# Optimization experiments

Measured on AMD Instinct MI355X. Metric: run time of the kernel, lower is better.

## Reference

```python
import jax, jax.numpy as jnp
import numpy as np

NODE_DIM = 64
DEPTH = 2
N = 50000          # node_size
DEG = 24           # average degree
E = N * DEG        # triple_size = 1.2M edges
R = 500            # rel_size
FEAT = NODE_DIM * (DEPTH + 1)  # 192


def _l2norm(x, eps=1e-12):
    # torch F.normalize(p=2): x / max(||x||, eps)
    n = jnp.sqrt(jnp.sum(x * x, axis=-1, keepdims=True))
    return x / jnp.maximum(n, eps)


def setup_inputs() -> dict:
    key = jax.random.key(0)
    ks = jax.random.split(key, 8)
    features = jax.random.normal(ks[0], (N, NODE_DIM), jnp.float32)
    rel_emb = jax.random.normal(ks[1], (R, NODE_DIM), jnp.float32)
    # duplicate-free edge list, rows sorted (matches a coalesced sparse adj)
    rows = jnp.repeat(jnp.arange(N, dtype=jnp.int32), DEG)
    offs = jnp.tile(1 + jnp.arange(DEG, dtype=jnp.int32) * 7, N)
    cols = (rows + offs) % N
    adj = jnp.stack([rows, cols])  # [2, E]
    # sparse [E, R] triple->relation matrix: one relation per triple
    r_index = jnp.stack([jnp.arange(E, dtype=jnp.int32),
                         jax.random.randint(ks[2], (E,), 0, R, jnp.int32)])
    r_val = jax.random.uniform(ks[3], (E,), jnp.float32, 0.5, 1.5)
    # params (xavier-ish scales)
    proxy = jax.random.normal(ks[4], (64, FEAT), jnp.float32) * (1.0 / np.sqrt(FEAT))
    gate_w = jax.random.normal(ks[5], (FEAT, FEAT), jnp.float32) * (1.0 / np.sqrt(FEAT))
    gate_b = jnp.zeros((FEAT,), jnp.float32)
    attn_kernels = jax.random.normal(ks[6], (DEPTH, NODE_DIM), jnp.float32) * 0.1
    return {"features": features, "rel_emb": rel_emb, "proxy": proxy,
            "gate_w": gate_w, "gate_b": gate_b, "attn_kernels": attn_kernels,
            "adj": adj, "r_index": r_index, "r_val": r_val,
            "triple_size": E, "rel_size": R, "node_size": N}


def reference(features, rel_emb, proxy, gate_w, gate_b, attn_kernels,
              adj, r_index, r_val, triple_size, rel_size, node_size):
    feats = jnp.tanh(features)
    outs = [feats]
    dst = adj[0]  # rows: softmax / scatter-sum segment ids
    src = adj[1]  # cols: neighbor gather ids
    for l in range(attn_kernels.shape[0]):
        neighs = feats[src]                                  # [E, d] gather
        # sparse.mm(tri_rel, rel_emb): sum_k r_val * rel_emb[rel_id] per triple
        tri_rel = jax.ops.segment_sum(r_val[:, None] * rel_emb[r_index[1]],
                                      r_index[0], num_segments=triple_size)
        tri_rel = _l2norm(tri_rel)                           # [E, d]
        # relational reflection: h - 2 <h, r> r
        neighs = neighs - 2.0 * jnp.sum(neighs * tri_rel, axis=1, keepdims=True) * tri_rel
        att = jnp.einsum('ed,d->e', tri_rel, attn_kernels[l])  # [E]
        # sparse softmax over rows of adjacency (segment softmax over dst)
        m = jax.ops.segment_max(att, dst, num_segments=node_size)
        ex = jnp.exp(att - m[dst])
        denom = jax.ops.segment_sum(ex, dst, num_segments=node_size)
        w = ex / denom[dst]
        new_f = jax.ops.segment_sum(neighs * w[:, None], dst, num_segments=node_size)
        feats = jnp.tanh(new_f)
        outs.append(feats)
    outputs = jnp.concatenate(outs, axis=-1)                 # [N, feat]
    proxy_att = jax.nn.softmax(_l2norm(outputs) @ _l2norm(proxy).T, axis=-1)
    proxy_feature = outputs - proxy_att @ proxy
    gate = jax.nn.sigmoid(proxy_feature @ gate_w.T + gate_b)
    return gate * outputs + (1.0 - gate) * proxy_feature
```

## Files before the change

### kernel.cpp

```cpp
#include <hip/hip_runtime.h>
#include <hip/hip_bf16.h>
#include <cstdint>
#include <cstddef>

#define N_NODES 50000
#define DEG     24
#define NEDGE   (N_NODES*DEG)
#define RSZ     500
#define NDIM    64
#define FEATD   192

#define LSTR    200

#define LGRID   1568
#define LCHUNK  196

typedef short bf16x8 __attribute__((ext_vector_type(8)));
typedef float f32x4  __attribute__((ext_vector_type(4)));

__device__ __forceinline__ unsigned short f2bf(float f) {
    unsigned u = __builtin_bit_cast(unsigned, f);
    unsigned r = (u + 0x7fffu + ((u >> 16) & 1u)) >> 16;
    return (unsigned short)r;
}
__device__ __forceinline__ float bf2f(unsigned short s) {
    unsigned u = ((unsigned)s) << 16;
    return __builtin_bit_cast(float, u);
}
__device__ __forceinline__ float lo16(unsigned u) {
    return __builtin_bit_cast(float, u << 16);
}
__device__ __forceinline__ float hi16(unsigned u) {
    return __builtin_bit_cast(float, u & 0xFFFF0000u);
}
__device__ __forceinline__ float fast_tanh(float x) {
    float e = __expf(2.f * x);
    return 1.f - 2.f / (e + 1.f);
}

__global__ __launch_bounds__(256) void k_prep(const float* __restrict__ features,
                                              const float* __restrict__ rel_emb,
                                              const float* __restrict__ attn_k,
                                              const float* __restrict__ proxy,
                                              const float* __restrict__ gate_w,
                                              const int* __restrict__ src,
                                              const int* __restrict__ rel,
                                              unsigned short* __restrict__ fin0,
                                              float* __restrict__ reln,
                                              float* __restrict__ expdot,
                                              float* __restrict__ pninv,
                                              unsigned short* __restrict__ B1,
                                              unsigned short* __restrict__ B2,
                                              unsigned short* __restrict__ B3,
                                              unsigned int* __restrict__ pedge) {
    int b = blockIdx.x;
    if (b < 3125) {
        int t = b * 256 + threadIdx.x;
        int idx4 = t * 4;
        float4 f = *reinterpret_cast<const float4*>(features + idx4);
        uint2 w;
        w.x = (unsigned)f2bf(fast_tanh(f.x)) | ((unsigned)f2bf(fast_tanh(f.y)) << 16);
        w.y = (unsigned)f2bf(fast_tanh(f.z)) | ((unsigned)f2bf(fast_tanh(f.w)) << 16);
        *reinterpret_cast<uint2*>(fin0 + idx4) = w;
    } else if (b < 3250) {
        int lane = threadIdx.x & 63;
        int row = (b - 3125) * 4 + (threadIdx.x >> 6);
        float v = rel_emb[row * 64 + lane];
        float ss = v * v;
        for (int m = 1; m < 64; m <<= 1) ss += __shfl_xor(ss, m);
        float inv = 1.f / fmaxf(sqrtf(ss), 1e-12f);
        float rn = v * inv;
        reln[row * 64 + lane] = rn;
        float d0 = rn * attn_k[lane];
        float d1 = rn * attn_k[64 + lane];
        for (int m = 1; m < 64; m <<= 1) { d0 += __shfl_xor(d0, m); d1 += __shfl_xor(d1, m); }
        if (lane == 0) { expdot[row] = __expf(d0); expdot[RSZ + row] = __expf(d1); }
    } else if (b < 3266) {
        int lane = threadIdx.x & 63;
        int row = (b - 3250) * 4 + (threadIdx.x >> 6);
        const float* p = proxy + (size_t)row * FEATD;
        float a = p[lane], bb = p[64 + lane], c = p[128 + lane];
        float ss = a * a + bb * bb + c * c;
        for (int m = 1; m < 64; m <<= 1) ss += __shfl_xor(ss, m);
        if (lane == 0) pninv[row] = 1.f / fmaxf(sqrtf(ss), 1e-12f);
    } else if (b < 3506) {
        int idx = (b - 3266) * 256 + threadIdx.x;
        int j = idx & 7, lane = (idx >> 3) & 63;
        int t = idx >> 9;
        int lane16 = lane & 15, quad = lane >> 4;
        if (t < 24) {
            int kt = t >> 2, nt = t & 3;
            int k = kt * 32 + quad * 8 + j, n = nt * 16 + lane16;
            B1[idx] = f2bf(proxy[(size_t)n * FEATD + k]);
        } else if (t < 48) {
            int tt = t - 24, kt = tt / 12, nt = tt % 12;
            int k = kt * 32 + quad * 8 + j, n = nt * 16 + lane16;
            B2[idx - 12288] = f2bf(proxy[(size_t)k * FEATD + n]);
        } else {
            int tt = t - 48, kt = tt / 12, nt = tt % 12;
            int k = kt * 32 + quad * 8 + j, n = nt * 16 + lane16;
            B3[idx - 24576] = f2bf(gate_w[(size_t)n * FEATD + k]);
        }
    } else {
        int t = (b - 3506) * 256 + threadIdx.x;
        if (t < NEDGE / 4) {
            int4 s4 = *reinterpret_cast<const int4*>(src + t * 4);
            int4 r4 = *reinterpret_cast<const int4*>(rel + t * 4);
            uint4 o;
            o.x = (unsigned)s4.x | ((unsigned)r4.x << 16);
            o.y = (unsigned)s4.y | ((unsigned)r4.y << 16);
            o.z = (unsigned)s4.z | ((unsigned)r4.z << 16);
            o.w = (unsigned)s4.w | ((unsigned)r4.w << 16);
            *reinterpret_cast<uint4*>(pedge + t * 4) = o;
        }
    }
}

__global__ __launch_bounds__(256) void k_layer(const unsigned int* __restrict__ pedge,
                                               const float* __restrict__ reln,
                                               const float* __restrict__ expdot_l,
                                               const unsigned short* __restrict__ fin,
                                               unsigned short* __restrict__ fout) {
    int b = blockIdx.x;
    int lb = (b & 7) * LCHUNK + (b >> 3);
    int lane8 = threadIdx.x & 7;
    int node = lb * 32 + (threadIdx.x >> 3);
    if (node >= N_NODES) return;
    int ebase = node * DEG;
    unsigned pk[DEG];
#pragma unroll
    for (int k = 0; k < DEG; k++) pk[k] = pedge[ebase + k];
    float a0 = 0.f, a1 = 0.f, a2 = 0.f, a3 = 0.f;
    float a4 = 0.f, a5 = 0.f, a6 = 0.f, a7 = 0.f, den = 0.f;
#pragma unroll 4
    for (int k = 0; k < DEG; k++) {
        unsigned p = pk[k];
        int s = p & 0xFFFF;
        int r = p >> 16;
        float ex = expdot_l[r];
        const float* tp = reln + (size_t)r * 64 + lane8 * 8;
        float4 t0 = *reinterpret_cast<const float4*>(tp);
        float4 t1v = *reinterpret_cast<const float4*>(tp + 4);
        uint4 u = *reinterpret_cast<const uint4*>(fin + (size_t)s * 64 + lane8 * 8);
        float n0 = lo16(u.x), n1 = hi16(u.x), n2 = lo16(u.y), n3 = hi16(u.y);
        float n4 = lo16(u.z), n5 = hi16(u.z), n6 = lo16(u.w), n7 = hi16(u.w);
        float pd = t0.x * n0 + t0.y * n1 + t0.z * n2 + t0.w * n3
                 + t1v.x * n4 + t1v.y * n5 + t1v.z * n6 + t1v.w * n7;
        pd += __shfl_xor(pd, 1); pd += __shfl_xor(pd, 2); pd += __shfl_xor(pd, 4);
        float t1 = -2.f * pd * ex;
        a0 = fmaf(ex, n0, fmaf(t1, t0.x, a0));
        a1 = fmaf(ex, n1, fmaf(t1, t0.y, a1));
        a2 = fmaf(ex, n2, fmaf(t1, t0.z, a2));
        a3 = fmaf(ex, n3, fmaf(t1, t0.w, a3));
        a4 = fmaf(ex, n4, fmaf(t1, t1v.x, a4));
        a5 = fmaf(ex, n5, fmaf(t1, t1v.y, a5));
        a6 = fmaf(ex, n6, fmaf(t1, t1v.z, a6));
        a7 = fmaf(ex, n7, fmaf(t1, t1v.w, a7));
        den += ex;
    }
    float id = 1.f / den;
    uint4 w;
    w.x = (unsigned)f2bf(fast_tanh(a0 * id)) | ((unsigned)f2bf(fast_tanh(a1 * id)) << 16);
    w.y = (unsigned)f2bf(fast_tanh(a2 * id)) | ((unsigned)f2bf(fast_tanh(a3 * id)) << 16);
    w.z = (unsigned)f2bf(fast_tanh(a4 * id)) | ((unsigned)f2bf(fast_tanh(a5 * id)) << 16);
    w.w = (unsigned)f2bf(fast_tanh(a6 * id)) | ((unsigned)f2bf(fast_tanh(a7 * id)) << 16);
    *reinterpret_cast<uint4*>(fout + (size_t)node * 64 + lane8 * 8) = w;
}

__global__ __launch_bounds__(256) void k_gate(const unsigned short* __restrict__ fin0,
                                              const unsigned short* __restrict__ fin1,
                                              const unsigned short* __restrict__ fin2,
                                              const unsigned short* __restrict__ B1,
                                              const unsigned short* __restrict__ B2,
                                              const unsigned short* __restrict__ B3,
                                              const float* __restrict__ pninv,
                                              const float* __restrict__ gate_b,
                                              float* __restrict__ dout) {
    __shared__ unsigned short lds[4][16 * LSTR];
    int wv = threadIdx.x >> 6, lane = threadIdx.x & 63;
    int tile = blockIdx.x * 4 + wv;
    if (tile > N_NODES / 16 - 1) tile = N_NODES / 16 - 1;
    int row0 = tile * 16, lane16 = lane & 15, quad = lane >> 4;
    unsigned short* L = lds[wv];
    const unsigned short* fsel[3] = {fin0, fin1, fin2};

    float oreg[12][4];
#pragma unroll
    for (int nt = 0; nt < 12; nt++) {
        const unsigned short* f = fsel[nt >> 2];
#pragma unroll
        for (int r = 0; r < 4; r++)
            oreg[nt][r] = bf2f(f[(size_t)(row0 + quad * 4 + r) * 64 + (nt & 3) * 16 + lane16]);
    }

    bf16x8 af[6];
    float ss = 0.f;
#pragma unroll
    for (int kt = 0; kt < 6; kt++) {
        const unsigned short* f = fsel[kt >> 1];
        bf16x8 a = *reinterpret_cast<const bf16x8*>(f + (size_t)(row0 + lane16) * 64 + (kt & 1) * 32 + quad * 8);
        af[kt] = a;
#pragma unroll
        for (int i = 0; i < 8; i++) {
            float v = bf2f((unsigned short)a[i]);
            ss = fmaf(v, v, ss);
        }
    }
    ss += __shfl_xor(ss, 16); ss += __shfl_xor(ss, 32);
    float inv = 1.f / fmaxf(sqrtf(ss), 1e-12f);
    float pni[4];
#pragma unroll
    for (int nt = 0; nt < 4; nt++) pni[nt] = pninv[nt * 16 + lane16];
    f32x4 acc4[4];
#pragma unroll
    for (int nt = 0; nt < 4; nt++) acc4[nt] = (f32x4){0.f, 0.f, 0.f, 0.f};
#pragma unroll
    for (int kt = 0; kt < 6; kt++) {
#pragma unroll
        for (int nt = 0; nt < 4; nt++) {
            bf16x8 bfr = *reinterpret_cast<const bf16x8*>(B1 + ((size_t)(kt * 4 + nt) * 64 + lane) * 8);
            acc4[nt] = __builtin_amdgcn_mfma_f32_16x16x32_bf16(af[kt], bfr, acc4[nt], 0, 0, 0);
        }
    }
#pragma unroll
    for (int r = 0; r < 4; r++) {
        int rowloc = quad * 4 + r;
        float invr = __shfl(inv, rowloc);
        float e0 = __expf(acc4[0][r] * invr * pni[0]);
        float e1 = __expf(acc4[1][r] * invr * pni[1]);
        float e2 = __expf(acc4[2][r] * invr * pni[2]);
        float e3 = __expf(acc4[3][r] * invr * pni[3]);
        float s = e0 + e1 + e2 + e3;
        s += __shfl_xor(s, 1); s += __shfl_xor(s, 2);
        s += __shfl_xor(s, 4); s += __shfl_xor(s, 8);
        float rs = 1.f / s;
        L[rowloc * LSTR + lane16]      = f2bf(e0 * rs);
        L[rowloc * LSTR + 16 + lane16] = f2bf(e1 * rs);
        L[rowloc * LSTR + 32 + lane16] = f2bf(e2 * rs);
        L[rowloc * LSTR + 48 + lane16] = f2bf(e3 * rs);
    }
    __threadfence_block();

    f32x4 acc[12];
#pragma unroll
    for (int nt = 0; nt < 12; nt++) acc[nt] = (f32x4){0.f, 0.f, 0.f, 0.f};
#pragma unroll
    for (int kt = 0; kt < 2; kt++) {
        bf16x8 a = *reinterpret_cast<const bf16x8*>(L + lane16 * LSTR + kt * 32 + quad * 8);
#pragma unroll
        for (int nt = 0; nt < 12; nt++) {
            bf16x8 bfr = *reinterpret_cast<const bf16x8*>(B2 + ((size_t)(kt * 12 + nt) * 64 + lane) * 8);
            acc[nt] = __builtin_amdgcn_mfma_f32_16x16x32_bf16(a, bfr, acc[nt], 0, 0, 0);
        }
    }
    __threadfence_block();
#pragma unroll
    for (int nt = 0; nt < 12; nt++) {
#pragma unroll
        for (int r = 0; r < 4; r++) {
            int rowloc = quad * 4 + r;
            L[rowloc * LSTR + nt * 16 + lane16] = f2bf(oreg[nt][r] - acc[nt][r]);
        }
    }
    __threadfence_block();

#pragma unroll
    for (int nt = 0; nt < 12; nt++) acc[nt] = (f32x4){0.f, 0.f, 0.f, 0.f};
#pragma unroll
    for (int kt = 0; kt < 6; kt++) {
        bf16x8 a = *reinterpret_cast<const bf16x8*>(L + lane16 * LSTR + kt * 32 + quad * 8);
#pragma unroll
        for (int nt = 0; nt < 12; nt++) {
            bf16x8 bfr = *reinterpret_cast<const bf16x8*>(B3 + ((size_t)(kt * 12 + nt) * 64 + lane) * 8);
            acc[nt] = __builtin_amdgcn_mfma_f32_16x16x32_bf16(a, bfr, acc[nt], 0, 0, 0);
        }
    }

#pragma unroll
    for (int nt = 0; nt < 12; nt++) {
        float bias = gate_b[nt * 16 + lane16];
#pragma unroll
        for (int r = 0; r < 4; r++) {
            int rowloc = quad * 4 + r;
            size_t idx = (size_t)(row0 + rowloc) * FEATD + nt * 16 + lane16;
            float z = acc[nt][r] + bias;
            float g = 1.f / (1.f + __expf(-z));
            float pf = bf2f(L[rowloc * LSTR + nt * 16 + lane16]);
            dout[idx] = pf + g * (oreg[nt][r] - pf);
        }
    }
}

extern "C" void kernel_launch(void* const* d_in, const int* in_sizes, int n_in,
                              void* d_out, int out_size, void* d_ws, size_t ws_size,
                              hipStream_t stream) {
    (void)in_sizes; (void)n_in; (void)out_size; (void)ws_size;
    const float* features = (const float*)d_in[0];
    const float* rel_emb  = (const float*)d_in[1];
    const float* proxy    = (const float*)d_in[2];
    const float* gate_w   = (const float*)d_in[3];
    const float* gate_b   = (const float*)d_in[4];
    const float* attn_k   = (const float*)d_in[5];
    const int*   adj      = (const int*)d_in[6];
    const int*   r_index  = (const int*)d_in[7];

    unsigned short* fin0 = (unsigned short*)d_ws;
    unsigned short* fin1 = fin0 + (size_t)N_NODES * 64;
    unsigned short* fin2 = fin1 + (size_t)N_NODES * 64;
    float* reln    = (float*)(fin2 + (size_t)N_NODES * 64);
    float* expdot  = reln + RSZ * 64;
    float* pninv   = expdot + 2 * RSZ;
    unsigned short* B1 = (unsigned short*)(pninv + 64);
    unsigned short* B2 = B1 + 12288;
    unsigned short* B3 = B2 + 12288;
    unsigned int* pedge = (unsigned int*)(B3 + 36864);

    const int* src = adj + NEDGE;
    const int* rel = r_index + NEDGE;

    k_prep  <<<dim3(4678), dim3(256), 0, stream>>>(features, rel_emb, attn_k, proxy, gate_w,
                                                   src, rel, fin0, reln, expdot,
                                                   pninv, B1, B2, B3, pedge);
    k_layer <<<dim3(LGRID), dim3(256), 0, stream>>>(pedge, reln, expdot,       fin0, fin1);
    k_layer <<<dim3(LGRID), dim3(256), 0, stream>>>(pedge, reln, expdot + RSZ, fin1, fin2);
    k_gate  <<<dim3(782),  dim3(256), 0, stream>>>(fin0, fin1, fin2, B1, B2, B3, pninv,
                                                   gate_b, (float*)d_out);
}
```

Baseline: 186.8 us.

## Stage normalized relation table in LDS with persistent 1024-thread layer blocks

Adds a layer kernel that loads the 500x64 normalized relation embeddings and per-relation exp weights into shared memory (~138KB, padded stride) once per block, then processes 196 nodes per block with 256 large blocks. Relation lookups per edge hit LDS instead of global/L2. The large LDS allocation limits occupancy to one block per CU and adds a per-block table load; falls back to the old kernel if the attribute set fails.

New measurement: 183.0 us. 2.0% less time.

```diff
diff --git a/kernel.cpp b/kernel.cpp
--- a/kernel.cpp
+++ b/kernel.cpp
@@ -14,6 +14,10 @@
 
 #define LGRID   1568
 #define LCHUNK  196
+
+#define NPB     196
+#define SREL_STRIDE 68
+#define LAYER_LDS_BYTES ((RSZ*SREL_STRIDE + RSZ) * 4)
 
 typedef short bf16x8 __attribute__((ext_vector_type(8)));
 typedef float f32x4  __attribute__((ext_vector_type(4)));
@@ -116,6 +120,72 @@
     }
 }
 
+__global__ __launch_bounds__(1024) void k_layer_lds(const unsigned int* __restrict__ pedge,
+                                                    const float* __restrict__ reln,
+                                                    const float* __restrict__ expdot_l,
+                                                    const unsigned short* __restrict__ fin,
+                                                    unsigned short* __restrict__ fout) {
+    extern __shared__ float smem[];
+    float* srel = smem;
+    float* sexp = smem + RSZ * SREL_STRIDE;
+    {
+        const float4* s4 = reinterpret_cast<const float4*>(reln);
+        for (int i = threadIdx.x; i < RSZ * 16; i += 1024) {
+            int row = i >> 4, c4 = i & 15;
+            *reinterpret_cast<float4*>(srel + row * SREL_STRIDE + c4 * 4) = s4[i];
+        }
+        for (int i = threadIdx.x; i < RSZ; i += 1024) sexp[i] = expdot_l[i];
+    }
+    __syncthreads();
+    int b = blockIdx.x;
+    int lb = (b & 7) * 32 + (b >> 3);
+    int base = lb * NPB;
+    int lane8 = threadIdx.x & 7;
+    for (int local = threadIdx.x >> 3; local < NPB; local += 128) {
+        int node = base + local;
+        if (node >= N_NODES) break;
+        int ebase = node * DEG;
+        unsigned pk[DEG];
+#pragma unroll
+        for (int k = 0; k < DEG; k++) pk[k] = pedge[ebase + k];
+        float a0 = 0.f, a1 = 0.f, a2 = 0.f, a3 = 0.f;
+        float a4 = 0.f, a5 = 0.f, a6 = 0.f, a7 = 0.f, den = 0.f;
+#pragma unroll 2
+        for (int k = 0; k < DEG; k++) {
+            unsigned p = pk[k];
+            int s = p & 0xFFFF;
+            int r = p >> 16;
+            float ex = sexp[r];
+            const float* tp = srel + r * SREL_STRIDE + lane8 * 8;
+            float4 t0 = *reinterpret_cast<const float4*>(tp);
+            float4 t1v = *reinterpret_cast<const float4*>(tp + 4);
+            uint4 u = *reinterpret_cast<const uint4*>(fin + (size_t)s * 64 + lane8 * 8);
+            float n0 = lo16(u.x), n1 = hi16(u.x), n2 = lo16(u.y), n3 = hi16(u.y);
+            float n4 = lo16(u.z), n5 = hi16(u.z), n6 = lo16(u.w), n7 = hi16(u.w);
+            float pd = t0.x * n0 + t0.y * n1 + t0.z * n2 + t0.w * n3
+                     + t1v.x * n4 + t1v.y * n5 + t1v.z * n6 + t1v.w * n7;
+            pd += __shfl_xor(pd, 1); pd += __shfl_xor(pd, 2); pd += __shfl_xor(pd, 4);
+            float t1 = -2.f * pd * ex;
+            a0 = fmaf(ex, n0, fmaf(t1, t0.x, a0));
+            a1 = fmaf(ex, n1, fmaf(t1, t0.y, a1));
+            a2 = fmaf(ex, n2, fmaf(t1, t0.z, a2));
+            a3 = fmaf(ex, n3, fmaf(t1, t0.w, a3));
+            a4 = fmaf(ex, n4, fmaf(t1, t1v.x, a4));
+            a5 = fmaf(ex, n5, fmaf(t1, t1v.y, a5));
+            a6 = fmaf(ex, n6, fmaf(t1, t1v.z, a6));
+            a7 = fmaf(ex, n7, fmaf(t1, t1v.w, a7));
+            den += ex;
+        }
+        float id = 1.f / den;
+        uint4 w;
+        w.x = (unsigned)f2bf(fast_tanh(a0 * id)) | ((unsigned)f2bf(fast_tanh(a1 * id)) << 16);
+        w.y = (unsigned)f2bf(fast_tanh(a2 * id)) | ((unsigned)f2bf(fast_tanh(a3 * id)) << 16);
+        w.z = (unsigned)f2bf(fast_tanh(a4 * id)) | ((unsigned)f2bf(fast_tanh(a5 * id)) << 16);
+        w.w = (unsigned)f2bf(fast_tanh(a6 * id)) | ((unsigned)f2bf(fast_tanh(a7 * id)) << 16);
+        *reinterpret_cast<uint4*>(fout + (size_t)node * 64 + lane8 * 8) = w;
+    }
+}
+
 __global__ __launch_bounds__(256) void k_layer(const unsigned int* __restrict__ pedge,
                                                const float* __restrict__ reln,
                                                const float* __restrict__ expdot_l,
@@ -318,11 +388,24 @@
     const int* src = adj + NEDGE;
     const int* rel = r_index + NEDGE;
 
+    static int lds_mode = -1;
+    if (lds_mode < 0) {
+        hipError_t e = hipFuncSetAttribute((const void*)k_layer_lds,
+                                           hipFuncAttributeMaxDynamicSharedMemorySize,
+                                           LAYER_LDS_BYTES);
+        lds_mode = (e == hipSuccess) ? 1 : 0;
+    }
+
     k_prep  <<<dim3(4678), dim3(256), 0, stream>>>(features, rel_emb, attn_k, proxy, gate_w,
                                                    src, rel, fin0, reln, expdot,
                                                    pninv, B1, B2, B3, pedge);
-    k_layer <<<dim3(LGRID), dim3(256), 0, stream>>>(pedge, reln, expdot,       fin0, fin1);
-    k_layer <<<dim3(LGRID), dim3(256), 0, stream>>>(pedge, reln, expdot + RSZ, fin1, fin2);
+    if (lds_mode == 1) {
+        k_layer_lds <<<dim3(256), dim3(1024), LAYER_LDS_BYTES, stream>>>(pedge, reln, expdot,       fin0, fin1);
+        k_layer_lds <<<dim3(256), dim3(1024), LAYER_LDS_BYTES, stream>>>(pedge, reln, expdot + RSZ, fin1, fin2);
+    } else {
+        k_layer <<<dim3(LGRID), dim3(256), 0, stream>>>(pedge, reln, expdot,       fin0, fin1);
+        k_layer <<<dim3(LGRID), dim3(256), 0, stream>>>(pedge, reln, expdot + RSZ, fin1, fin2);
+    }
     k_gate  <<<dim3(782),  dim3(256), 0, stream>>>(fin0, fin1, fin2, B1, B2, B3, pninv,
                                                    gate_b, (float*)d_out);
 }
```

## Remap blocks XCD-aware across prep and gate kernels and batch B-fragment loads

Applied to the files above, without the earlier changes.

The features-to-bf16 part of the prep kernel now handles 32 nodes per block with a block-index swizzle of the form (b&7)*chunk + (b>>3). The edge-packing part and the gate kernel use the same kind of remap, so that blocks scheduled on the same XCD handle contiguous node ranges, matching the layer kernel's chunking and improving L2 locality. The gate kernel gets a launch-bounds occupancy hint, and its B-fragment global loads are batched before the MFMA chains to expose memory-level parallelism. The grids are resized to fit the new mapping. The batched loads raise register pressure, and the occupancy hint may force spills.

Result: no change. 184.3 us (-1.4%).

```diff
diff --git a/kernel.cpp b/kernel.cpp
--- a/kernel.cpp
+++ b/kernel.cpp
@@ -54,17 +54,24 @@
                                               unsigned short* __restrict__ B3,
                                               unsigned int* __restrict__ pedge) {
     int b = blockIdx.x;
-    if (b < 3125) {
-        int t = b * 256 + threadIdx.x;
-        int idx4 = t * 4;
-        float4 f = *reinterpret_cast<const float4*>(features + idx4);
-        uint2 w;
-        w.x = (unsigned)f2bf(fast_tanh(f.x)) | ((unsigned)f2bf(fast_tanh(f.y)) << 16);
-        w.y = (unsigned)f2bf(fast_tanh(f.z)) | ((unsigned)f2bf(fast_tanh(f.w)) << 16);
-        *reinterpret_cast<uint2*>(fin0 + idx4) = w;
-    } else if (b < 3250) {
+    if (b < 1568) {
+        int lb = (b & 7) * LCHUNK + (b >> 3);
+        int node = lb * 32 + ((int)threadIdx.x >> 3);
+        if (node < N_NODES) {
+            int d0 = ((int)threadIdx.x & 7) * 8;
+            const float* fp = features + (size_t)node * 64 + d0;
+            float4 f0 = *reinterpret_cast<const float4*>(fp);
+            float4 f1 = *reinterpret_cast<const float4*>(fp + 4);
+            uint4 w;
+            w.x = (unsigned)f2bf(fast_tanh(f0.x)) | ((unsigned)f2bf(fast_tanh(f0.y)) << 16);
+            w.y = (unsigned)f2bf(fast_tanh(f0.z)) | ((unsigned)f2bf(fast_tanh(f0.w)) << 16);
+            w.z = (unsigned)f2bf(fast_tanh(f1.x)) | ((unsigned)f2bf(fast_tanh(f1.y)) << 16);
+            w.w = (unsigned)f2bf(fast_tanh(f1.z)) | ((unsigned)f2bf(fast_tanh(f1.w)) << 16);
+            *reinterpret_cast<uint4*>(fin0 + (size_t)node * 64 + d0) = w;
+        }
+    } else if (b < 1693) {
         int lane = threadIdx.x & 63;
-        int row = (b - 3125) * 4 + (threadIdx.x >> 6);
+        int row = (b - 1568) * 4 + (threadIdx.x >> 6);
         float v = rel_emb[row * 64 + lane];
         float ss = v * v;
         for (int m = 1; m < 64; m <<= 1) ss += __shfl_xor(ss, m);
@@ -75,16 +82,16 @@
         float d1 = rn * attn_k[64 + lane];
         for (int m = 1; m < 64; m <<= 1) { d0 += __shfl_xor(d0, m); d1 += __shfl_xor(d1, m); }
         if (lane == 0) { expdot[row] = __expf(d0); expdot[RSZ + row] = __expf(d1); }
-    } else if (b < 3266) {
+    } else if (b < 1709) {
         int lane = threadIdx.x & 63;
-        int row = (b - 3250) * 4 + (threadIdx.x >> 6);
+        int row = (b - 1693) * 4 + (threadIdx.x >> 6);
         const float* p = proxy + (size_t)row * FEATD;
         float a = p[lane], bb = p[64 + lane], c = p[128 + lane];
         float ss = a * a + bb * bb + c * c;
         for (int m = 1; m < 64; m <<= 1) ss += __shfl_xor(ss, m);
         if (lane == 0) pninv[row] = 1.f / fmaxf(sqrtf(ss), 1e-12f);
-    } else if (b < 3506) {
-        int idx = (b - 3266) * 256 + threadIdx.x;
+    } else if (b < 1949) {
+        int idx = (b - 1709) * 256 + threadIdx.x;
         int j = idx & 7, lane = (idx >> 3) & 63;
         int t = idx >> 9;
         int lane16 = lane & 15, quad = lane >> 4;
@@ -102,7 +109,9 @@
             B3[idx - 24576] = f2bf(gate_w[(size_t)n * FEATD + k]);
         }
     } else {
-        int t = (b - 3506) * 256 + threadIdx.x;
+        int bb = b - 1949;
+        int lb = (bb & 7) * 147 + (bb >> 3);
+        int t = lb * 256 + (int)threadIdx.x;
         if (t < NEDGE / 4) {
             int4 s4 = *reinterpret_cast<const int4*>(src + t * 4);
             int4 r4 = *reinterpret_cast<const int4*>(rel + t * 4);
@@ -167,18 +176,20 @@
     *reinterpret_cast<uint4*>(fout + (size_t)node * 64 + lane8 * 8) = w;
 }
 
-__global__ __launch_bounds__(256) void k_gate(const unsigned short* __restrict__ fin0,
-                                              const unsigned short* __restrict__ fin1,
-                                              const unsigned short* __restrict__ fin2,
-                                              const unsigned short* __restrict__ B1,
-                                              const unsigned short* __restrict__ B2,
-                                              const unsigned short* __restrict__ B3,
-                                              const float* __restrict__ pninv,
-                                              const float* __restrict__ gate_b,
-                                              float* __restrict__ dout) {
+__global__ __launch_bounds__(256, 3) void k_gate(const unsigned short* __restrict__ fin0,
+                                                 const unsigned short* __restrict__ fin1,
+                                                 const unsigned short* __restrict__ fin2,
+                                                 const unsigned short* __restrict__ B1,
+                                                 const unsigned short* __restrict__ B2,
+                                                 const unsigned short* __restrict__ B3,
+                                                 const float* __restrict__ pninv,
+                                                 const float* __restrict__ gate_b,
+                                                 float* __restrict__ dout) {
     __shared__ unsigned short lds[4][16 * LSTR];
     int wv = threadIdx.x >> 6, lane = threadIdx.x & 63;
-    int tile = blockIdx.x * 4 + wv;
+    int b = blockIdx.x;
+    int lb = (b & 7) * 98 + (b >> 3);
+    int tile = lb * 4 + wv;
     if (tile > N_NODES / 16 - 1) tile = N_NODES / 16 - 1;
     int row0 = tile * 16, lane16 = lane & 15, quad = lane >> 4;
     unsigned short* L = lds[wv];
@@ -215,12 +226,18 @@
 #pragma unroll
     for (int nt = 0; nt < 4; nt++) acc4[nt] = (f32x4){0.f, 0.f, 0.f, 0.f};
 #pragma unroll
-    for (int kt = 0; kt < 6; kt++) {
-#pragma unroll
-        for (int nt = 0; nt < 4; nt++) {
-            bf16x8 bfr = *reinterpret_cast<const bf16x8*>(B1 + ((size_t)(kt * 4 + nt) * 64 + lane) * 8);
-            acc4[nt] = __builtin_amdgcn_mfma_f32_16x16x32_bf16(af[kt], bfr, acc4[nt], 0, 0, 0);
-        }
+    for (int ktp = 0; ktp < 3; ktp++) {
+        bf16x8 bb[8];
+#pragma unroll
+        for (int h = 0; h < 2; h++)
+#pragma unroll
+            for (int nt = 0; nt < 4; nt++)
+                bb[h * 4 + nt] = *reinterpret_cast<const bf16x8*>(B1 + ((size_t)((ktp * 2 + h) * 4 + nt) * 64 + lane) * 8);
+#pragma unroll
+        for (int h = 0; h < 2; h++)
+#pragma unroll
+            for (int nt = 0; nt < 4; nt++)
+                acc4[nt] = __builtin_amdgcn_mfma_f32_16x16x32_bf16(af[ktp * 2 + h], bb[h * 4 + nt], acc4[nt], 0, 0, 0);
     }
 #pragma unroll
     for (int r = 0; r < 4; r++) {
@@ -247,11 +264,13 @@
 #pragma unroll
     for (int kt = 0; kt < 2; kt++) {
         bf16x8 a = *reinterpret_cast<const bf16x8*>(L + lane16 * LSTR + kt * 32 + quad * 8);
-#pragma unroll
-        for (int nt = 0; nt < 12; nt++) {
-            bf16x8 bfr = *reinterpret_cast<const bf16x8*>(B2 + ((size_t)(kt * 12 + nt) * 64 + lane) * 8);
-            acc[nt] = __builtin_amdgcn_mfma_f32_16x16x32_bf16(a, bfr, acc[nt], 0, 0, 0);
-        }
+        bf16x8 bb[12];
+#pragma unroll
+        for (int nt = 0; nt < 12; nt++)
+            bb[nt] = *reinterpret_cast<const bf16x8*>(B2 + ((size_t)(kt * 12 + nt) * 64 + lane) * 8);
+#pragma unroll
+        for (int nt = 0; nt < 12; nt++)
+            acc[nt] = __builtin_amdgcn_mfma_f32_16x16x32_bf16(a, bb[nt], acc[nt], 0, 0, 0);
     }
     __threadfence_block();
 #pragma unroll
@@ -269,11 +288,13 @@
 #pragma unroll
     for (int kt = 0; kt < 6; kt++) {
         bf16x8 a = *reinterpret_cast<const bf16x8*>(L + lane16 * LSTR + kt * 32 + quad * 8);
-#pragma unroll
-        for (int nt = 0; nt < 12; nt++) {
-            bf16x8 bfr = *reinterpret_cast<const bf16x8*>(B3 + ((size_t)(kt * 12 + nt) * 64 + lane) * 8);
-            acc[nt] = __builtin_amdgcn_mfma_f32_16x16x32_bf16(a, bfr, acc[nt], 0, 0, 0);
-        }
+        bf16x8 bb[12];
+#pragma unroll
+        for (int nt = 0; nt < 12; nt++)
+            bb[nt] = *reinterpret_cast<const bf16x8*>(B3 + ((size_t)(kt * 12 + nt) * 64 + lane) * 8);
+#pragma unroll
+        for (int nt = 0; nt < 12; nt++)
+            acc[nt] = __builtin_amdgcn_mfma_f32_16x16x32_bf16(a, bb[nt], acc[nt], 0, 0, 0);
     }
 
 #pragma unroll
@@ -318,11 +339,11 @@
     const int* src = adj + NEDGE;
     const int* rel = r_index + NEDGE;
 
-    k_prep  <<<dim3(4678), dim3(256), 0, stream>>>(features, rel_emb, attn_k, proxy, gate_w,
+    k_prep  <<<dim3(3125), dim3(256), 0, stream>>>(features, rel_emb, attn_k, proxy, gate_w,
                                                    src, rel, fin0, reln, expdot,
                                                    pninv, B1, B2, B3, pedge);
     k_layer <<<dim3(LGRID), dim3(256), 0, stream>>>(pedge, reln, expdot,       fin0, fin1);
     k_layer <<<dim3(LGRID), dim3(256), 0, stream>>>(pedge, reln, expdot + RSZ, fin1, fin2);
-    k_gate  <<<dim3(782),  dim3(256), 0, stream>>>(fin0, fin1, fin2, B1, B2, B3, pninv,
+    k_gate  <<<dim3(784),  dim3(256), 0, stream>>>(fin0, fin1, fin2, B1, B2, B3, pninv,
                                                    gate_b, (float*)d_out);
 }
```

## Fuse both GNN layers into one persistent kernel with a grid barrier

Applied to the files above, without the earlier changes.

Merges the two per-layer launches into one persistent kernel of 784 blocks. Each block handles two node groups per layer, and a global atomic-counter barrier sits between the layers. The barrier counter is zeroed in the prep kernel. The gate kernel also batches its B-fragment loads ahead of the MFMA chains and gets launch-bound hints, meant to trim launch gaps and hide load latency. In exchange it relies on all 784 blocks being co-resident for the spin barrier (deadlock risk otherwise) and gives up the parallel slack of the larger grid.

Measured after the change: 370.0 us. +98.0%, slower.

```diff
diff --git a/kernel.cpp b/kernel.cpp
--- a/kernel.cpp
+++ b/kernel.cpp
@@ -12,7 +12,7 @@
 
 #define LSTR    200
 
-#define LGRID   1568
+#define NBLK    784
 #define LCHUNK  196
 
 typedef short bf16x8 __attribute__((ext_vector_type(8)));
@@ -52,8 +52,10 @@
                                               unsigned short* __restrict__ B1,
                                               unsigned short* __restrict__ B2,
                                               unsigned short* __restrict__ B3,
-                                              unsigned int* __restrict__ pedge) {
+                                              unsigned int* __restrict__ pedge,
+                                              unsigned int* __restrict__ bar) {
     int b = blockIdx.x;
+    if (b == 0 && threadIdx.x < 2) bar[threadIdx.x] = 0;
     if (b < 3125) {
         int t = b * 256 + threadIdx.x;
         int idx4 = t * 4;
@@ -116,15 +118,15 @@
     }
 }
 
-__global__ __launch_bounds__(256) void k_layer(const unsigned int* __restrict__ pedge,
-                                               const float* __restrict__ reln,
-                                               const float* __restrict__ expdot_l,
-                                               const unsigned short* __restrict__ fin,
-                                               unsigned short* __restrict__ fout) {
-    int b = blockIdx.x;
-    int lb = (b & 7) * LCHUNK + (b >> 3);
-    int lane8 = threadIdx.x & 7;
-    int node = lb * 32 + (threadIdx.x >> 3);
+__device__ __forceinline__ void layer_pass(int lg, int tid,
+                                           const unsigned int* __restrict__ pedge,
+                                           const float* __restrict__ reln,
+                                           const float* __restrict__ expdot_l,
+                                           const unsigned short* __restrict__ fin,
+                                           unsigned short* __restrict__ fout) {
+    int lb = (lg & 7) * LCHUNK + (lg >> 3);
+    int lane8 = tid & 7;
+    int node = lb * 32 + (tid >> 3);
     if (node >= N_NODES) return;
     int ebase = node * DEG;
     unsigned pk[DEG];
@@ -167,15 +169,38 @@
     *reinterpret_cast<uint4*>(fout + (size_t)node * 64 + lane8 * 8) = w;
 }
 
-__global__ __launch_bounds__(256) void k_gate(const unsigned short* __restrict__ fin0,
-                                              const unsigned short* __restrict__ fin1,
-                                              const unsigned short* __restrict__ fin2,
-                                              const unsigned short* __restrict__ B1,
-                                              const unsigned short* __restrict__ B2,
-                                              const unsigned short* __restrict__ B3,
-                                              const float* __restrict__ pninv,
-                                              const float* __restrict__ gate_b,
-                                              float* __restrict__ dout) {
+__global__ __launch_bounds__(256, 4) void k_layers(const unsigned int* __restrict__ pedge,
+                                                   const float* __restrict__ reln,
+                                                   const float* __restrict__ expdot,
+                                                   const unsigned short* __restrict__ fin0,
+                                                   unsigned short* __restrict__ fin1,
+                                                   unsigned short* __restrict__ fin2,
+                                                   unsigned int* bar) {
+    int tid = threadIdx.x;
+    int b = blockIdx.x;
+    layer_pass(b,        tid, pedge, reln, expdot, fin0, fin1);
+    layer_pass(b + NBLK, tid, pedge, reln, expdot, fin0, fin1);
+    __threadfence();
+    __syncthreads();
+    if (tid == 0) {
+        atomicAdd(bar, 1u);
+        while (atomicAdd(bar, 0u) < (unsigned)NBLK) __builtin_amdgcn_s_sleep(2);
+    }
+    __syncthreads();
+    __threadfence();
+    layer_pass(b,        tid, pedge, reln, expdot + RSZ, fin1, fin2);
+    layer_pass(b + NBLK, tid, pedge, reln, expdot + RSZ, fin1, fin2);
+}
+
+__global__ __launch_bounds__(256, 3) void k_gate(const unsigned short* __restrict__ fin0,
+                                                 const unsigned short* __restrict__ fin1,
+                                                 const unsigned short* __restrict__ fin2,
+                                                 const unsigned short* __restrict__ B1,
+                                                 const unsigned short* __restrict__ B2,
+                                                 const unsigned short* __restrict__ B3,
+                                                 const float* __restrict__ pninv,
+                                                 const float* __restrict__ gate_b,
+                                                 float* __restrict__ dout) {
     __shared__ unsigned short lds[4][16 * LSTR];
     int wv = threadIdx.x >> 6, lane = threadIdx.x & 63;
     int tile = blockIdx.x * 4 + wv;
@@ -215,12 +240,18 @@
 #pragma unroll
     for (int nt = 0; nt < 4; nt++) acc4[nt] = (f32x4){0.f, 0.f, 0.f, 0.f};
 #pragma unroll
-    for (int kt = 0; kt < 6; kt++) {
-#pragma unroll
-        for (int nt = 0; nt < 4; nt++) {
-            bf16x8 bfr = *reinterpret_cast<const bf16x8*>(B1 + ((size_t)(kt * 4 + nt) * 64 + lane) * 8);
-            acc4[nt] = __builtin_amdgcn_mfma_f32_16x16x32_bf16(af[kt], bfr, acc4[nt], 0, 0, 0);
-        }
+    for (int ktp = 0; ktp < 3; ktp++) {
+        bf16x8 bb[8];
+#pragma unroll
+        for (int h = 0; h < 2; h++)
+#pragma unroll
+            for (int nt = 0; nt < 4; nt++)
+                bb[h * 4 + nt] = *reinterpret_cast<const bf16x8*>(B1 + ((size_t)((ktp * 2 + h) * 4 + nt) * 64 + lane) * 8);
+#pragma unroll
+        for (int h = 0; h < 2; h++)
+#pragma unroll
+            for (int nt = 0; nt < 4; nt++)
+                acc4[nt] = __builtin_amdgcn_mfma_f32_16x16x32_bf16(af[ktp * 2 + h], bb[h * 4 + nt], acc4[nt], 0, 0, 0);
     }
 #pragma unroll
     for (int r = 0; r < 4; r++) {
@@ -247,11 +278,13 @@
 #pragma unroll
     for (int kt = 0; kt < 2; kt++) {
         bf16x8 a = *reinterpret_cast<const bf16x8*>(L + lane16 * LSTR + kt * 32 + quad * 8);
-#pragma unroll
-        for (int nt = 0; nt < 12; nt++) {
-            bf16x8 bfr = *reinterpret_cast<const bf16x8*>(B2 + ((size_t)(kt * 12 + nt) * 64 + lane) * 8);
-            acc[nt] = __builtin_amdgcn_mfma_f32_16x16x32_bf16(a, bfr, acc[nt], 0, 0, 0);
-        }
+        bf16x8 bb[12];
+#pragma unroll
+        for (int nt = 0; nt < 12; nt++)
+            bb[nt] = *reinterpret_cast<const bf16x8*>(B2 + ((size_t)(kt * 12 + nt) * 64 + lane) * 8);
+#pragma unroll
+        for (int nt = 0; nt < 12; nt++)
+            acc[nt] = __builtin_amdgcn_mfma_f32_16x16x32_bf16(a, bb[nt], acc[nt], 0, 0, 0);
     }
     __threadfence_block();
 #pragma unroll
@@ -269,11 +302,13 @@
 #pragma unroll
     for (int kt = 0; kt < 6; kt++) {
         bf16x8 a = *reinterpret_cast<const bf16x8*>(L + lane16 * LSTR + kt * 32 + quad * 8);
-#pragma unroll
-        for (int nt = 0; nt < 12; nt++) {
-            bf16x8 bfr = *reinterpret_cast<const bf16x8*>(B3 + ((size_t)(kt * 12 + nt) * 64 + lane) * 8);
-            acc[nt] = __builtin_amdgcn_mfma_f32_16x16x32_bf16(a, bfr, acc[nt], 0, 0, 0);
-        }
+        bf16x8 bb[12];
+#pragma unroll
+        for (int nt = 0; nt < 12; nt++)
+            bb[nt] = *reinterpret_cast<const bf16x8*>(B3 + ((size_t)(kt * 12 + nt) * 64 + lane) * 8);
+#pragma unroll
+        for (int nt = 0; nt < 12; nt++)
+            acc[nt] = __builtin_amdgcn_mfma_f32_16x16x32_bf16(a, bb[nt], acc[nt], 0, 0, 0);
     }
 
 #pragma unroll
@@ -314,15 +349,15 @@
     unsigned short* B2 = B1 + 12288;
     unsigned short* B3 = B2 + 12288;
     unsigned int* pedge = (unsigned int*)(B3 + 36864);
+    unsigned int* bar   = pedge + NEDGE;
 
     const int* src = adj + NEDGE;
     const int* rel = r_index + NEDGE;
 
-    k_prep  <<<dim3(4678), dim3(256), 0, stream>>>(features, rel_emb, attn_k, proxy, gate_w,
-                                                   src, rel, fin0, reln, expdot,
-                                                   pninv, B1, B2, B3, pedge);
-    k_layer <<<dim3(LGRID), dim3(256), 0, stream>>>(pedge, reln, expdot,       fin0, fin1);
-    k_layer <<<dim3(LGRID), dim3(256), 0, stream>>>(pedge, reln, expdot + RSZ, fin1, fin2);
-    k_gate  <<<dim3(782),  dim3(256), 0, stream>>>(fin0, fin1, fin2, B1, B2, B3, pninv,
-                                                   gate_b, (float*)d_out);
-}
+    k_prep   <<<dim3(4678), dim3(256), 0, stream>>>(features, rel_emb, attn_k, proxy, gate_w,
+                                                    src, rel, fin0, reln, expdot,
+                                                    pninv, B1, B2, B3, pedge, bar);
+    k_layers <<<dim3(NBLK), dim3(256), 0, stream>>>(pedge, reln, expdot, fin0, fin1, fin2, bar);
+    k_gate   <<<dim3(782),  dim3(256), 0, stream>>>(fin0, fin1, fin2, B1, B2, B3, pninv,
+                                                    gate_b, (float*)d_out);
+}
```
